# Optimization experiments

Hardware: AMD Instinct MI355X
Metric: run time of the kernel (lower is better)

The kernel has to match this reference:

```python
import jax, jax.numpy as jnp
import numpy as np

DEPTH = 12
NODE_SIZE = 64
IN_SCALE = 1.0
SCALE = 0.1
IN_W = 1.8
SIZE = 2 ** DEPTH - 1          # 4095 total nodes
REST = SIZE - 1                # 4094 non-root nodes
M_BATCH = 128


def setup_inputs() -> dict:
    key = jax.random.key(0)
    k1, k2, k3 = jax.random.split(key, 3)
    weights = IN_W + 1e-4 * jax.random.normal(k1, (SIZE,), dtype=jnp.float32)
    noise_root = jax.random.normal(k2, (M_BATCH, NODE_SIZE, 1), dtype=jnp.float32)
    noise_rest = jax.random.normal(k3, (M_BATCH, NODE_SIZE, REST), dtype=jnp.float32)
    return {"weights": weights, "noise_root": noise_root, "noise_rest": noise_rest, "M": M_BATCH}


def reference(weights, noise_root, noise_rest, M):
    # Root: Normal(0, in_scale).rsample((M, node_size, 1))
    root = IN_SCALE * noise_root                      # (M, node, 1)
    samples_levels = [root]
    m_levels = []
    scale_levels = []
    off = 0
    for d in range(1, DEPTH):
        n = 2 ** d
        w = jax.nn.sigmoid(weights[off:off + n])       # (n,)
        parent = jnp.arange(n) // 2                    # half-index parent lookup
        m = w[None, None, :] * samples_levels[-1][:, :, parent]   # (M, node, n)
        sc = jnp.broadcast_to(((1.0 - w) * SCALE)[None, None, :], m.shape)
        samp = m + sc * noise_rest[:, :, off:off + n]  # reparameterized rsample
        samples_levels.append(samp)
        m_levels.append(m)
        scale_levels.append(sc)
        off += n
    samples = jnp.concatenate(samples_levels[::-1], axis=2)  # (M, node, 4095)
    ms = jnp.concatenate(m_levels[::-1], axis=2)              # (M, node, 4094)
    scales = jnp.concatenate(scale_levels[::-1], axis=2)      # (M, node, 4094)
    return samples, ms, scales
```

## Files before the change

kernel.cpp:

```cpp
#include <hip/hip_runtime.h>


constexpr int   kRows  = 8192;
constexpr float kScale = 0.1f;

__device__ __align__(16) float2 g_tab[4096];

__global__ __launch_bounds__(256) void lgt_precompute(
    const float* __restrict__ weights)
{
    int t = blockIdx.x * 256 + threadIdx.x;
    if (t < 4094) {
        int d = 31 - __clz(t + 2);
        int c = t + 4098 - 3 * (1 << d);
        float w = 1.0f / (1.0f + __expf(-weights[t]));
        g_tab[c] = make_float2(w, (1.0f - w) * kScale);
    }
}

__device__ __forceinline__ void lgkm_barrier() {
    __builtin_amdgcn_sched_barrier(0);
    asm volatile("s_waitcnt lgkmcnt(0)" ::: "memory");
    __builtin_amdgcn_s_barrier();
    __builtin_amdgcn_sched_barrier(0);
}

__global__ __launch_bounds__(256) void lgt_main(
    const float* __restrict__ noise_root,
    const float* __restrict__ noise_rest,
    float* __restrict__ samples,
    float* __restrict__ ms,
    float* __restrict__ scales)
{
    __shared__ float s[4096];

    const int row = blockIdx.x;
    const int tid = threadIdx.x;
    const float* __restrict__ nr = noise_rest + (size_t)row * 4094;
    float* __restrict__ sr = samples + (size_t)row * 4095;
    float* __restrict__ mr = ms      + (size_t)row * 4094;
    float* __restrict__ cr = scales  + (size_t)row * 4094;

    const float nzs = nr[tid];
    const float nz8 = nr[254 + tid];
    float nz9[2], nz10[4], nz11[8];
    #pragma unroll
    for (int k = 0; k < 2; ++k) nz9[k]  = nr[510  + tid + (k << 8)];
    #pragma unroll
    for (int k = 0; k < 4; ++k) nz10[k] = nr[1022 + tid + (k << 8)];
    #pragma unroll
    for (int k = 0; k < 8; ++k) nz11[k] = nr[2046 + tid + (k << 8)];
    const float rootv = noise_root[row];

    if (tid == 0) { s[4094] = rootv; sr[4094] = rootv; }
    lgkm_barrier();

    #pragma unroll
    for (int d = 1; d <= 7; ++d) {
        const int off = (1 << d) - 2;
        const int n   = 1 << d;
        const int colbase = 4096 - (n << 1);
        if (tid >= off && tid < off + n) {
            const int c = colbase + (tid - off);
            const float2 t2 = g_tab[c];
            const float  p  = s[(c >> 1) + 2048];
            const float  mv = t2.x * p;
            const float  v  = fmaf(t2.y, nzs, mv);
            s[c] = v;
            sr[c] = v; mr[c] = mv; cr[c] = t2.y;
        }
        lgkm_barrier();
    }

    {
        const int c = 3584 + tid;
        const float2 t2 = g_tab[c];
        const float  p  = s[(c >> 1) + 2048];
        const float  mv = t2.x * p;
        const float  v  = fmaf(t2.y, nz8, mv);
        s[c] = v;
        sr[c] = v; mr[c] = mv; cr[c] = t2.y;
    }
    lgkm_barrier();

    #pragma unroll
    for (int k = 0; k < 2; ++k) {
        const int c = 3072 + tid + (k << 8);
        const float2 t2 = g_tab[c];
        const float  p  = s[(c >> 1) + 2048];
        const float  mv = t2.x * p;
        const float  v  = fmaf(t2.y, nz9[k], mv);
        s[c] = v;
        sr[c] = v; mr[c] = mv; cr[c] = t2.y;
    }
    lgkm_barrier();

    #pragma unroll
    for (int k = 0; k < 4; ++k) {
        const int c = 2048 + tid + (k << 8);
        const float2 t2 = g_tab[c];
        const float  p  = s[(c >> 1) + 2048];
        const float  mv = t2.x * p;
        const float  v  = fmaf(t2.y, nz10[k], mv);
        s[c] = v;
        sr[c] = v; mr[c] = mv; cr[c] = t2.y;
    }
    lgkm_barrier();

    #pragma unroll
    for (int k = 0; k < 8; ++k) {
        const int c = tid + (k << 8);
        const float2 t2 = g_tab[c];
        const float  p  = s[(c >> 1) + 2048];
        const float  mv = t2.x * p;
        const float  v  = fmaf(t2.y, nz11[k], mv);
        sr[c] = v; mr[c] = mv; cr[c] = t2.y;
    }
}

extern "C" void kernel_launch(void* const* d_in, const int* in_sizes, int n_in,
                              void* d_out, int out_size, void* d_ws, size_t ws_size,
                              hipStream_t stream)
{
    const float* weights    = (const float*)d_in[0];
    const float* noise_root = (const float*)d_in[1];
    const float* noise_rest = (const float*)d_in[2];

    float* out     = (float*)d_out;
    float* samples = out;
    float* ms      = samples + (size_t)kRows * 4095;
    float* scales  = ms      + (size_t)kRows * 4094;

    lgt_precompute<<<(4094 + 255) / 256, 256, 0, stream>>>(weights);
    lgt_main<<<kRows, 256, 0, stream>>>(noise_root, noise_rest,
                                        samples, ms, scales);
}
```

Measured before the change: 121.9 us.

## Give each thread its own subtree for the last four levels, vectorize I/O

The last four tree levels are no longer computed level by level through shared memory. Each thread now owns one level-7 node and computes its whole subtree (2, 4, then 8 descendants) in registers, so three block barriers and most shared-memory traffic go away. Noise loads and the sample, mean and scale stores become contiguous vector accesses per thread. Some of these vectors are unaligned because rows are 4094 or 4095 floats long, and the per-thread strided access means fewer consecutive addresses per instruction across a wavefront.

```diff
diff --git a/kernel.cpp b/kernel.cpp
--- a/kernel.cpp
+++ b/kernel.cpp
@@ -3,6 +3,11 @@
 
 constexpr int   kRows  = 8192;
 constexpr float kScale = 0.1f;
+
+typedef float f4_ __attribute__((ext_vector_type(4)));
+typedef float f2_ __attribute__((ext_vector_type(2)));
+typedef f4_ f4u __attribute__((aligned(4)));
+typedef f2_ f2u __attribute__((aligned(4)));
 
 __device__ __align__(16) float2 g_tab[4096];
 
@@ -32,7 +37,7 @@
     float* __restrict__ ms,
     float* __restrict__ scales)
 {
-    __shared__ float s[4096];
+    __shared__ float sL[256];
 
     const int row = blockIdx.x;
     const int tid = threadIdx.x;
@@ -42,79 +47,99 @@
     float* __restrict__ cr = scales  + (size_t)row * 4094;
 
     const float nzs = nr[tid];
-    const float nz8 = nr[254 + tid];
-    float nz9[2], nz10[4], nz11[8];
+    const float n8  = nr[254 + tid];
+    const f2_  n9   = *(const f2_*)(nr + 510 + 2 * tid);
+    const f2_  nA0  = *(const f2_*)(nr + 1022 + 4 * tid);
+    const f2_  nA1  = *(const f2_*)(nr + 1022 + 4 * tid + 2);
+    f2_ nL[4];
     #pragma unroll
-    for (int k = 0; k < 2; ++k) nz9[k]  = nr[510  + tid + (k << 8)];
-    #pragma unroll
-    for (int k = 0; k < 4; ++k) nz10[k] = nr[1022 + tid + (k << 8)];
-    #pragma unroll
-    for (int k = 0; k < 8; ++k) nz11[k] = nr[2046 + tid + (k << 8)];
+    for (int k = 0; k < 4; ++k)
+        nL[k] = *(const f2_*)(nr + 2046 + 8 * tid + 2 * k);
     const float rootv = noise_root[row];
 
-    if (tid == 0) { s[4094] = rootv; sr[4094] = rootv; }
+    if (tid == 0) { sL[254] = rootv; sr[4094] = rootv; }
     lgkm_barrier();
 
     #pragma unroll
     for (int d = 1; d <= 7; ++d) {
-        const int off = (1 << d) - 2;
-        const int n   = 1 << d;
+        const int off     = (1 << d) - 2;
+        const int n       = 1 << d;
         const int colbase = 4096 - (n << 1);
         if (tid >= off && tid < off + n) {
             const int c = colbase + (tid - off);
             const float2 t2 = g_tab[c];
-            const float  p  = s[(c >> 1) + 2048];
+            const float  p  = sL[(c >> 1) - 1792];
             const float  mv = t2.x * p;
             const float  v  = fmaf(t2.y, nzs, mv);
-            s[c] = v;
+            sL[c - 3840] = v;
             sr[c] = v; mr[c] = mv; cr[c] = t2.y;
         }
         lgkm_barrier();
     }
 
+    const float a7 = sL[tid >> 1];
+
+    const float2 t8 = g_tab[3584 + tid];
+    const float  m8 = t8.x * a7;
+    const float  v8 = fmaf(t8.y, n8, m8);
+    sr[3584 + tid] = v8; mr[3584 + tid] = m8; cr[3584 + tid] = t8.y;
+
+    const f4_ t9 = *(const f4_*)(&g_tab[3072 + 2 * tid]);
+    const float m90 = t9.x * v8, m91 = t9.z * v8;
+    const float v90 = fmaf(t9.y, n9.x, m90);
+    const float v91 = fmaf(t9.w, n9.y, m91);
     {
-        const int c = 3584 + tid;
-        const float2 t2 = g_tab[c];
-        const float  p  = s[(c >> 1) + 2048];
-        const float  mv = t2.x * p;
-        const float  v  = fmaf(t2.y, nz8, mv);
-        s[c] = v;
-        sr[c] = v; mr[c] = mv; cr[c] = t2.y;
+        f2_ sv; sv.x = v90; sv.y = v91;
+        f2_ mv; mv.x = m90; mv.y = m91;
+        f2_ cv; cv.x = t9.y; cv.y = t9.w;
+        *(f2u*)(sr + 3072 + 2 * tid) = sv;
+        *(f2_*)(mr + 3072 + 2 * tid) = mv;
+        *(f2_*)(cr + 3072 + 2 * tid) = cv;
     }
-    lgkm_barrier();
 
-    #pragma unroll
-    for (int k = 0; k < 2; ++k) {
-        const int c = 3072 + tid + (k << 8);
-        const float2 t2 = g_tab[c];
-        const float  p  = s[(c >> 1) + 2048];
-        const float  mv = t2.x * p;
-        const float  v  = fmaf(t2.y, nz9[k], mv);
-        s[c] = v;
-        sr[c] = v; mr[c] = mv; cr[c] = t2.y;
+    const f4_ tA = *(const f4_*)(&g_tab[2048 + 4 * tid]);
+    const f4_ tB = *(const f4_*)(&g_tab[2048 + 4 * tid + 2]);
+    const float mA0 = tA.x * v90, mA1 = tA.z * v90;
+    const float mB0 = tB.x * v91, mB1 = tB.z * v91;
+    const float vA0 = fmaf(tA.y, nA0.x, mA0);
+    const float vA1 = fmaf(tA.w, nA0.y, mA1);
+    const float vB0 = fmaf(tB.y, nA1.x, mB0);
+    const float vB1 = fmaf(tB.w, nA1.y, mB1);
+    {
+        f4_ sv; sv.x = vA0; sv.y = vA1; sv.z = vB0; sv.w = vB1;
+        f4_ mv; mv.x = mA0; mv.y = mA1; mv.z = mB0; mv.w = mB1;
+        f4_ cv; cv.x = tA.y; cv.y = tA.w; cv.z = tB.y; cv.w = tB.w;
+        *(f4u*)(sr + 2048 + 4 * tid) = sv;
+        *(f4u*)(mr + 2048 + 4 * tid) = mv;
+        *(f4u*)(cr + 2048 + 4 * tid) = cv;
     }
-    lgkm_barrier();
 
+    const float pv0 = vA0, pv1 = vA1, pv2 = vB0, pv3 = vB1;
+    float sv[8], mv[8], cv[8];
     #pragma unroll
     for (int k = 0; k < 4; ++k) {
-        const int c = 2048 + tid + (k << 8);
-        const float2 t2 = g_tab[c];
-        const float  p  = s[(c >> 1) + 2048];
-        const float  mv = t2.x * p;
-        const float  v  = fmaf(t2.y, nz10[k], mv);
-        s[c] = v;
-        sr[c] = v; mr[c] = mv; cr[c] = t2.y;
+        const f4_  t = *(const f4_*)(&g_tab[8 * tid + 2 * k]);
+        const float p = (k == 0) ? pv0 : (k == 1) ? pv1 : (k == 2) ? pv2 : pv3;
+        const float m0 = t.x * p, m1 = t.z * p;
+        sv[2 * k]     = fmaf(t.y, nL[k].x, m0);
+        sv[2 * k + 1] = fmaf(t.w, nL[k].y, m1);
+        mv[2 * k] = m0; mv[2 * k + 1] = m1;
+        cv[2 * k] = t.y; cv[2 * k + 1] = t.w;
     }
-    lgkm_barrier();
-
-    #pragma unroll
-    for (int k = 0; k < 8; ++k) {
-        const int c = tid + (k << 8);
-        const float2 t2 = g_tab[c];
-        const float  p  = s[(c >> 1) + 2048];
-        const float  mv = t2.x * p;
-        const float  v  = fmaf(t2.y, nz11[k], mv);
-        sr[c] = v; mr[c] = mv; cr[c] = t2.y;
+    {
+        f4_ a, b;
+        a.x = sv[0]; a.y = sv[1]; a.z = sv[2]; a.w = sv[3];
+        b.x = sv[4]; b.y = sv[5]; b.z = sv[6]; b.w = sv[7];
+        *(f4u*)(sr + 8 * tid)     = a;
+        *(f4u*)(sr + 8 * tid + 4) = b;
+        a.x = mv[0]; a.y = mv[1]; a.z = mv[2]; a.w = mv[3];
+        b.x = mv[4]; b.y = mv[5]; b.z = mv[6]; b.w = mv[7];
+        *(f4u*)(mr + 8 * tid)     = a;
+        *(f4u*)(mr + 8 * tid + 4) = b;
+        a.x = cv[0]; a.y = cv[1]; a.z = cv[2]; a.w = cv[3];
+        b.x = cv[4]; b.y = cv[5]; b.z = cv[6]; b.w = cv[7];
+        *(f4u*)(cr + 8 * tid)     = a;
+        *(f4u*)(cr + 8 * tid + 4) = b;
     }
 }
 
```

Result: no change. 120.3 us, median of 2 (-1.3%).
